# Kernel optimization log

Measured on AMD Instinct MI355X. Metric: run time of the kernel, lower is better.

## Reference

```python
import jax, jax.numpy as jnp
import numpy as np

H = W = 256
C = 256
N_ROIS = 2000
POOL = 7


def setup_inputs() -> dict:
    key = jax.random.key(0)
    kf, kw, kh, kx, ky = jax.random.split(key, 5)
    feature_map = jax.random.normal(kf, (1, H, W, C), dtype=jnp.float32)
    # ROI format: (batch_idx, x, y, w, h), integer pixel coords, in-bounds
    w = jax.random.randint(kw, (N_ROIS,), 8, 65)
    h = jax.random.randint(kh, (N_ROIS,), 8, 65)
    x = jax.random.randint(kx, (N_ROIS,), 0, W - 64)
    y = jax.random.randint(ky, (N_ROIS,), 0, H - 64)
    rois = jnp.stack([jnp.zeros_like(x), x, y, w, h], axis=1).astype(jnp.int32)
    return {"feature_map": feature_map, "rois": rois, "pool_size": POOL}


def _axis_coords(start, length, pool_size):
    """Sample coords along one axis, matching tf.image.resize bilinear
    (half-pixel centers) applied to the crop [start, start+length).
    start, length: [N] int. Returns abs idx0, idx1 [N,P] int and frac [N,P]."""
    lf = length.astype(jnp.float32)
    # source coord within the crop for each output pixel
    f = (jnp.arange(pool_size, dtype=jnp.float32) + 0.5)[None, :] * (lf / pool_size)[:, None] - 0.5
    f = jnp.clip(f, 0.0, (lf - 1.0)[:, None])
    i0 = jnp.floor(f).astype(jnp.int32)
    i1 = jnp.minimum(i0 + 1, (length - 1)[:, None])
    frac = f - i0.astype(jnp.float32)
    return start[:, None] + i0, start[:, None] + i1, frac


def _roi_pool(feature_map, rois, pool_size):
    fm = feature_map[0]                      # [H, W, C]
    x, y, w, h = rois[:, 1], rois[:, 2], rois[:, 3], rois[:, 4]
    y0, y1, fy = _axis_coords(y, h, pool_size)   # [N, P]
    x0, x1, fx = _axis_coords(x, w, pool_size)   # [N, P]

    def g(yi, xi):  # gather -> [N, P, P, C]
        return fm[yi[:, :, None], xi[:, None, :], :]

    fx_ = fx[:, None, :, None]
    fy_ = fy[:, :, None, None]
    top = g(y0, x0) * (1.0 - fx_) + g(y0, x1) * fx_
    bot = g(y1, x0) * (1.0 - fx_) + g(y1, x1) * fx_
    return top * (1.0 - fy_) + bot * fy_     # [N, P, P, C]


def reference(feature_map, rois, pool_size):
    return _roi_pool(feature_map, rois, pool_size)
```

## Files before the change

### kernel.cpp

```cpp
#include <hip/hip_runtime.h>

#define FH 256
#define FW 256
#define FC 256
#define POOL 7
#define CPW 4

typedef float f32x4 __attribute__((ext_vector_type(4)));

__global__ __launch_bounds__(256) void roi_pool_kernel(
    const float* __restrict__ fm,
    const int*   __restrict__ rois,
    float*       __restrict__ out,
    int n_cells, int chunk)
{
    int b  = blockIdx.x;
    int lb = (b & 7) * chunk + (b >> 3);

    int lane = threadIdx.x & 63;
    int wave = threadIdx.x >> 6;
    int base_cell = __builtin_amdgcn_readfirstlane((lb * 4 + wave) * CPW);
    if (base_cell >= n_cells) return;

    f32x4 A[CPW], B[CPW], C[CPW], D[CPW];
    float WX[CPW], WY[CPW];

#pragma unroll
    for (int c = 0; c < CPW; ++c) {
        int cell = base_cell + c;
        int pi  = cell % POOL;
        int tmp = cell / POOL;
        int pj  = tmp % POOL;
        int roi = tmp / POOL;

        int rx = rois[roi * 5 + 1];
        int ry = rois[roi * 5 + 2];
        int rw = rois[roi * 5 + 3];
        int rh = rois[roi * 5 + 4];

        float lfh = (float)rh;
        float fy  = ((float)pj + 0.5f) * (lfh / (float)POOL) - 0.5f;
        fy = fminf(fmaxf(fy, 0.0f), lfh - 1.0f);
        int   j0 = (int)floorf(fy);
        int   j1 = min(j0 + 1, rh - 1);
        WY[c] = fy - (float)j0;
        int   y0 = ry + j0;
        int   y1 = ry + j1;

        float lfw = (float)rw;
        float fx  = ((float)pi + 0.5f) * (lfw / (float)POOL) - 0.5f;
        fx = fminf(fmaxf(fx, 0.0f), lfw - 1.0f);
        int   i0 = (int)floorf(fx);
        int   i1 = min(i0 + 1, rw - 1);
        WX[c] = fx - (float)i0;
        int   x0 = rx + i0;
        int   x1 = rx + i1;

        A[c] = *((const f32x4*)(fm + ((size_t)y0 * FW + x0) * FC) + lane);
        B[c] = *((const f32x4*)(fm + ((size_t)y0 * FW + x1) * FC) + lane);
        C[c] = *((const f32x4*)(fm + ((size_t)y1 * FW + x0) * FC) + lane);
        D[c] = *((const f32x4*)(fm + ((size_t)y1 * FW + x1) * FC) + lane);
    }

#pragma unroll
    for (int c = 0; c < CPW; ++c) {
        float wx = WX[c], wy = WY[c];
        float owx = 1.0f - wx, owy = 1.0f - wy;
        f32x4 r = (A[c] * owx + B[c] * wx) * owy
                + (C[c] * owx + D[c] * wx) * wy;
        f32x4* o = (f32x4*)(out + (size_t)(base_cell + c) * FC) + lane;
        __builtin_nontemporal_store(r, o);
    }
}

extern "C" void kernel_launch(void* const* d_in, const int* in_sizes, int n_in,
                              void* d_out, int out_size, void* d_ws, size_t ws_size,
                              hipStream_t stream) {
    const float* fm   = (const float*)d_in[0];
    const int*   rois = (const int*)d_in[1];
    float* out = (float*)d_out;

    int n_rois  = in_sizes[1] / 5;
    int n_cells = n_rois * POOL * POOL;
    int n_waves = (n_cells + CPW - 1) / CPW;
    int blocks  = (n_waves + 3) / 4;
    blocks      = (blocks + 7) & ~7;
    int chunk   = blocks / 8;

    roi_pool_kernel<<<blocks, 256, 0, stream>>>(fm, rois, out, n_cells, chunk);
}
```

Before: 183.1 us.

## Bucket-sort ROIs by spatial center so neighbouring blocks share feature-map reads

Adds a single-block counting-sort kernel that buckets ROIs by their center on a 16x16 spatial grid and writes a permutation to the workspace. The pooling kernel then walks ROIs in sorted order, reads the original ROI through the permutation, and scatters its output to the original position. The aim is better L2/MALL reuse of feature-map pixels across concurrently running blocks. In exchange it adds an extra serial kernel launch, an indirection load per cell, and a prefix scan done by one thread. The keys array is sized at 2048, so larger ROI counts would overflow it.

```diff
diff --git a/kernel.cpp b/kernel.cpp
--- a/kernel.cpp
+++ b/kernel.cpp
@@ -4,13 +4,48 @@
 #define FW 256
 #define FC 256
 #define POOL 7
+#define CELLS_PER_ROI (POOL * POOL)
 #define CPW 4
 
 typedef float f32x4 __attribute__((ext_vector_type(4)));
 
+#define N_BUCKETS 256
+__global__ __launch_bounds__(256) void roi_sort_kernel(
+    const int* __restrict__ rois, int* __restrict__ perm, int n_rois)
+{
+    __shared__ int hist[N_BUCKETS];
+    __shared__ int base[N_BUCKETS];
+    __shared__ unsigned char keys[2048];
+    int t = threadIdx.x;
+    if (t < N_BUCKETS) hist[t] = 0;
+    __syncthreads();
+    for (int i = t; i < n_rois; i += blockDim.x) {
+        int x = rois[i * 5 + 1], y = rois[i * 5 + 2];
+        int w = rois[i * 5 + 3], h = rois[i * 5 + 4];
+        int cx = x + (w >> 1), cy = y + (h >> 1);
+        int key = (((cy >> 4) & 15) << 4) | ((cx >> 4) & 15);
+        keys[i] = (unsigned char)key;
+        atomicAdd(&hist[key], 1);
+    }
+    __syncthreads();
+    if (t == 0) {
+        int acc = 0;
+        for (int b = 0; b < N_BUCKETS; ++b) { base[b] = acc; acc += hist[b]; }
+    }
+    __syncthreads();
+    if (t < N_BUCKETS) hist[t] = 0;
+    __syncthreads();
+    for (int i = t; i < n_rois; i += blockDim.x) {
+        int key = keys[i];
+        int pos = base[key] + atomicAdd(&hist[key], 1);
+        perm[pos] = i;
+    }
+}
+
 __global__ __launch_bounds__(256) void roi_pool_kernel(
     const float* __restrict__ fm,
     const int*   __restrict__ rois,
+    const int*   __restrict__ perm,
     float*       __restrict__ out,
     int n_cells, int chunk)
 {
@@ -24,14 +59,17 @@
 
     f32x4 A[CPW], B[CPW], C[CPW], D[CPW];
     float WX[CPW], WY[CPW];
+    int   OROI[CPW], SUB[CPW];
 
 #pragma unroll
     for (int c = 0; c < CPW; ++c) {
         int cell = base_cell + c;
-        int pi  = cell % POOL;
-        int tmp = cell / POOL;
-        int pj  = tmp % POOL;
-        int roi = tmp / POOL;
+        int sorted_pos = cell / CELLS_PER_ROI;
+        int sub        = cell % CELLS_PER_ROI;
+        int roi  = perm[sorted_pos];
+        OROI[c] = roi; SUB[c] = sub;
+        int pi = sub % POOL;
+        int pj = sub / POOL;
 
         int rx = rois[roi * 5 + 1];
         int ry = rois[roi * 5 + 2];
@@ -68,7 +106,8 @@
         float owx = 1.0f - wx, owy = 1.0f - wy;
         f32x4 r = (A[c] * owx + B[c] * wx) * owy
                 + (C[c] * owx + D[c] * wx) * wy;
-        f32x4* o = (f32x4*)(out + (size_t)(base_cell + c) * FC) + lane;
+        size_t ocell = (size_t)OROI[c] * CELLS_PER_ROI + SUB[c];
+        f32x4* o = (f32x4*)(out + ocell * FC) + lane;
         __builtin_nontemporal_store(r, o);
     }
 }
@@ -78,14 +117,17 @@
                               hipStream_t stream) {
     const float* fm   = (const float*)d_in[0];
     const int*   rois = (const int*)d_in[1];
-    float* out = (float*)d_out;
+    float* out  = (float*)d_out;
+    int*   perm = (int*)d_ws;
 
     int n_rois  = in_sizes[1] / 5;
-    int n_cells = n_rois * POOL * POOL;
+    int n_cells = n_rois * CELLS_PER_ROI;
     int n_waves = (n_cells + CPW - 1) / CPW;
     int blocks  = (n_waves + 3) / 4;
     blocks      = (blocks + 7) & ~7;
     int chunk   = blocks / 8;
 
-    roi_pool_kernel<<<blocks, 256, 0, stream>>>(fm, rois, out, n_cells, chunk);
+    roi_sort_kernel<<<1, 256, 0, stream>>>(rois, perm, n_rois);
+    roi_pool_kernel<<<blocks, 256, 0, stream>>>(fm, rois, perm, out,
+                                                n_cells, chunk);
 }
```

New measurement: 187.2 us. 1.02x slower.
